# Kernel tuning notes

Measured on AMD Instinct MI355X. Metric: run time of the kernel, lower is better.

The kernel has to match this reference:

```python
import jax, jax.numpy as jnp
import numpy as np

EMBED = 1024
HEADS = 16
HEAD_DIM = EMBED // HEADS
HIDDEN = 4 * EMBED
EPS = 1e-5


def setup_inputs() -> dict:
    key = jax.random.key(0)
    ks = jax.random.split(key, 9)
    s = lambda fan_in: 1.0 / np.sqrt(fan_in)
    inp = {
        "x": jax.random.normal(ks[0], (2, 2048, EMBED), dtype=jnp.float32),
        "ln1_w": jnp.ones((EMBED,), jnp.float32),
        "ln1_b": jnp.zeros((EMBED,), jnp.float32),
        "ln2_w": jnp.ones((EMBED,), jnp.float32),
        "ln2_b": jnp.zeros((EMBED,), jnp.float32),
        "qkv_w": jax.random.uniform(ks[1], (EMBED, 3 * EMBED), jnp.float32, -s(EMBED), s(EMBED)),
        "qkv_b": jax.random.uniform(ks[2], (3 * EMBED,), jnp.float32, -s(EMBED), s(EMBED)),
        "proj_w": jax.random.uniform(ks[3], (EMBED, EMBED), jnp.float32, -s(EMBED), s(EMBED)),
        "proj_b": jax.random.uniform(ks[4], (EMBED,), jnp.float32, -s(EMBED), s(EMBED)),
        "fc1_w": jax.random.uniform(ks[5], (EMBED, HIDDEN), jnp.float32, -s(EMBED), s(EMBED)),
        "fc1_b": jax.random.uniform(ks[6], (HIDDEN,), jnp.float32, -s(EMBED), s(EMBED)),
        "fc2_w": jax.random.uniform(ks[7], (HIDDEN, EMBED), jnp.float32, -s(HIDDEN), s(HIDDEN)),
        "fc2_b": jax.random.uniform(ks[8], (EMBED,), jnp.float32, -s(HIDDEN), s(HIDDEN)),
    }
    return inp


def _layernorm(x, w, b):
    mu = jnp.mean(x, axis=-1, keepdims=True)
    var = jnp.mean(jnp.square(x - mu), axis=-1, keepdims=True)
    return (x - mu) * jax.lax.rsqrt(var + EPS) * w + b


def _attn(x, qkv_w, qkv_b, proj_w, proj_b):
    B, N, C = x.shape
    qkv = x @ qkv_w + qkv_b                      # [B,N,3C]
    qkv = qkv.reshape(B, N, 3, HEADS, HEAD_DIM)
    q, k, v = qkv[:, :, 0], qkv[:, :, 1], qkv[:, :, 2]   # [B,N,H,D]
    scale = HEAD_DIM ** -0.5
    scores = jnp.einsum("bqhd,bkhd->bhqk", q, k) * scale  # [B,H,N,N]
    attn = jax.nn.softmax(scores, axis=-1)
    out = jnp.einsum("bhqk,bkhd->bqhd", attn, v).reshape(B, N, C)
    return out @ proj_w + proj_b


def _mlp(x, fc1_w, fc1_b, fc2_w, fc2_b):
    h = jax.nn.gelu(x @ fc1_w + fc1_b, approximate=False)
    return h @ fc2_w + fc2_b


def reference(x, ln1_w, ln1_b, ln2_w, ln2_b, qkv_w, qkv_b, proj_w, proj_b,
              fc1_w, fc1_b, fc2_w, fc2_b):
    # pre-norm transformer block (eval mode: dropout/drop_path are identity)
    x = x + _attn(_layernorm(x, ln1_w, ln1_b), qkv_w, qkv_b, proj_w, proj_b)
    x = x + _mlp(_layernorm(x, ln2_w, ln2_b), fc1_w, fc1_b, fc2_w, fc2_b)
    return x
```

## Files before the change

### kernel.cpp

```cpp
#include <hip/hip_runtime.h>
#include <hip/hip_bf16.h>

#define SEQ    2048
#define BATCH  2
#define MTOK   4096
#define EMBED  1024
#define HEADS  16
#define HDIM   64
#define QKV3   3072
#define FFN    4096

typedef __attribute__((ext_vector_type(8))) short bf16x8;
typedef __attribute__((ext_vector_type(4))) float f32x4;

static __device__ __forceinline__ unsigned short f2bf(float f) {
  union { float f; unsigned u; } x; x.f = f;
  unsigned r = x.u + 0x7FFFu + ((x.u >> 16) & 1u);
  return (unsigned short)(r >> 16);
}
static __device__ __forceinline__ float bf2f(unsigned short u) {
  union { unsigned u; float f; } x; x.u = ((unsigned)u) << 16; return x.f;
}
static __device__ __forceinline__ unsigned pk2bf(float a, float b) {
#if __has_builtin(__builtin_amdgcn_cvt_pk_bf16_f32)
  typedef __attribute__((ext_vector_type(2))) __bf16 bf16x2_t;
  union { bf16x2_t v; unsigned u; } x;
  x.v = __builtin_amdgcn_cvt_pk_bf16_f32(a, b);
  return x.u;
#else
  return ((unsigned)f2bf(a)) | (((unsigned)f2bf(b)) << 16);
#endif
}
static __device__ __forceinline__ float fexp2(float x) {
#if __has_builtin(__builtin_amdgcn_exp2f)
  return __builtin_amdgcn_exp2f(x);
#else
  return exp2f(x);
#endif
}
static __device__ __forceinline__ float frcp(float x) {
#if __has_builtin(__builtin_amdgcn_rcpf)
  return __builtin_amdgcn_rcpf(x);
#else
  return 1.0f / x;
#endif
}
static __device__ __forceinline__ float fgelu(float v) {
  float t = v * v;
  float z = v * __builtin_fmaf(-0.1029456f, t, -2.3022650687f);
  return v * frcp(1.0f + fexp2(z));
}

static __device__ __forceinline__ void gload16(const unsigned short* g, unsigned short* l) {
  __builtin_amdgcn_global_load_lds((const __attribute__((address_space(1))) void*)g,
                                   (__attribute__((address_space(3))) void*)l, 16, 0, 0);
}

struct TD { const float* W; unsigned short* T; int K, N, ntx, base; };
struct TD4 { TD d[4]; };

__global__ void transpose_all(TD4 td) {
  __shared__ float t[32][33];
  int bid = blockIdx.x;
  int i = 0;
  if (bid >= td.d[1].base) i = 1;
  if (bid >= td.d[2].base) i = 2;
  if (bid >= td.d[3].base) i = 3;
  const TD& D = td.d[i];
  int local = bid - D.base;
  int n0 = (local % D.ntx) * 32, k0 = (local / D.ntx) * 32;
  int tx = threadIdx.x, ty = threadIdx.y;
#pragma unroll
  for (int j = 0; j < 32; j += 8)
    t[ty + j][tx] = D.W[(size_t)(k0 + ty + j) * D.N + n0 + tx];
  __syncthreads();
#pragma unroll
  for (int j = 0; j < 32; j += 8)
    D.T[(size_t)(n0 + ty + j) * D.K + k0 + tx] = f2bf(t[tx][ty + j]);
}

__global__ __launch_bounds__(256) void ln_kernel(const float* __restrict__ in,
                                                 const float* __restrict__ w,
                                                 const float* __restrict__ b,
                                                 unsigned short* __restrict__ out) {
  __shared__ float sh[4];
  int row = blockIdx.x, tid = threadIdx.x;
  const float4 v = ((const float4*)(in + (size_t)row * EMBED))[tid];
  float s = v.x + v.y + v.z + v.w;
#pragma unroll
  for (int off = 32; off; off >>= 1) s += __shfl_xor(s, off);
  if ((tid & 63) == 0) sh[tid >> 6] = s;
  __syncthreads();
  float mean = (sh[0] + sh[1] + sh[2] + sh[3]) * (1.0f / EMBED);
  __syncthreads();
  float dx = v.x - mean, dy = v.y - mean, dz = v.z - mean, dw = v.w - mean;
  float q = dx * dx + dy * dy + dz * dz + dw * dw;
#pragma unroll
  for (int off = 32; off; off >>= 1) q += __shfl_xor(q, off);
  if ((tid & 63) == 0) sh[tid >> 6] = q;
  __syncthreads();
  float var = (sh[0] + sh[1] + sh[2] + sh[3]) * (1.0f / EMBED);
  float rs = rsqrtf(var + 1e-5f);
  const float4 wv = ((const float4*)w)[tid];
  const float4 bv = ((const float4*)b)[tid];
  ushort4 o;
  o.x = f2bf(dx * rs * wv.x + bv.x);
  o.y = f2bf(dy * rs * wv.y + bv.y);
  o.z = f2bf(dz * rs * wv.z + bv.z);
  o.w = f2bf(dw * rs * wv.w + bv.w);
  ((ushort4*)(out + (size_t)row * EMBED))[tid] = o;
}

template <int ACT, int OUTBF, int VSPLIT>
__global__ __launch_bounds__(256) void gemmBig(const unsigned short* __restrict__ A,
                                               const unsigned short* __restrict__ Wt,
                                               const float* __restrict__ bias,
                                               unsigned short* __restrict__ outB,
                                               float* __restrict__ outF,
                                               unsigned short* __restrict__ vT,
                                               int M, int N, int K, int nblk) {
  __shared__ __align__(16) unsigned short As[128 * 64];
  __shared__ __align__(16) unsigned short Bs[128 * 64];
  const int tid = threadIdx.x;
  const int wave = tid >> 6, lane = tid & 63;
  const int quad = lane >> 4, ml = lane & 15;
  const int wr = wave >> 1, wc = wave & 1;
  const int m0 = (blockIdx.x / nblk) * 128;
  const int n0 = (blockIdx.x % nblk) * 128;
  const int srow = lane >> 3;
  const int schunk = (lane & 7) ^ (srow & 7);
  const unsigned short* Ag = A + (size_t)(m0 + wave * 32 + srow) * K + schunk * 8;
  const unsigned short* Bg = Wt + (size_t)(n0 + wave * 32 + srow) * K + schunk * 8;
  unsigned short* AsW = &As[wave * 2048];
  unsigned short* BsW = &Bs[wave * 2048];
  f32x4 acc[4][4];
#pragma unroll
  for (int i = 0; i < 4; i++)
#pragma unroll
    for (int j = 0; j < 4; j++) acc[i][j] = (f32x4){0.f, 0.f, 0.f, 0.f};
  for (int k0 = 0; k0 < K; k0 += 64) {
    __syncthreads();
#pragma unroll
    for (int t = 0; t < 4; t++) {
      gload16(Ag + (size_t)(8 * t) * K, AsW + 512 * t);
      gload16(Bg + (size_t)(8 * t) * K, BsW + 512 * t);
    }
    Ag += 64; Bg += 64;
    __syncthreads();
#pragma unroll
    for (int kh = 0; kh < 2; kh++) {
      const int ch = ((kh * 4 + quad) ^ (ml & 7)) * 8;
      bf16x8 af[4], bfr[4];
#pragma unroll
      for (int mt = 0; mt < 4; mt++)
        af[mt] = *(const bf16x8*)&As[(wr * 64 + mt * 16 + ml) * 64 + ch];
#pragma unroll
      for (int nt = 0; nt < 4; nt++)
        bfr[nt] = *(const bf16x8*)&Bs[(wc * 64 + nt * 16 + ml) * 64 + ch];
#pragma unroll
      for (int mt = 0; mt < 4; mt++)
#pragma unroll
        for (int nt = 0; nt < 4; nt++)
          acc[mt][nt] = __builtin_amdgcn_mfma_f32_16x16x32_bf16(af[mt], bfr[nt], acc[mt][nt], 0, 0, 0);
    }
  }
#pragma unroll
  for (int mt = 0; mt < 4; mt++)
#pragma unroll
    for (int nt = 0; nt < 4; nt++) {
      const int col0 = n0 + wc * 64 + nt * 16;
      const int row0 = m0 + wr * 64 + mt * 16;
      if (VSPLIT && col0 >= 2 * EMBED) {
        const int b = row0 >> 11, tok0 = row0 & (SEQ - 1);
        const int h = (col0 - 2 * EMBED) >> 6;
        const int dl = ((col0 - 2 * EMBED) & 63) + ml;
        float bia = bias[col0 + ml];
        ushort4 o;
        o.x = f2bf(acc[mt][nt][0] + bia);
        o.y = f2bf(acc[mt][nt][1] + bia);
        o.z = f2bf(acc[mt][nt][2] + bia);
        o.w = f2bf(acc[mt][nt][3] + bia);
        *(ushort4*)(vT + (size_t)((b * 16 + h) * 64 + dl) * SEQ + tok0 + quad * 4) = o;
      } else {
#pragma unroll
        for (int r = 0; r < 4; r++) {
          int row = row0 + quad * 4 + r;
          int col = col0 + ml;
          float v = acc[mt][nt][r] + bias[col];
          if (ACT) v = fgelu(v);
          if (OUTBF)
            outB[(size_t)row * N + col] = f2bf(v);
          else
            outF[(size_t)row * N + col] = v;
        }
      }
    }
}

template <int RES, int OUTBF>
__global__ __launch_bounds__(256) void gemm64k(const unsigned short* __restrict__ A,
                                               const unsigned short* __restrict__ Wt,
                                               const float* __restrict__ bias,
                                               const float* __restrict__ res,
                                               unsigned short* __restrict__ outB,
                                               float* __restrict__ outF,
                                               int M, int N, int K, int nblk) {
  __shared__ __align__(16) unsigned short As[2][128 * 64];
  __shared__ __align__(16) unsigned short Bs[2][64 * 64];
  const int tid = threadIdx.x;
  const int wave = tid >> 6, lane = tid & 63;
  const int quad = lane >> 4, ml = lane & 15;
  const int wr = wave >> 1, wc = wave & 1;
  const int xcd = blockIdx.x & 7, idx = blockIdx.x >> 3;
  const int mPerXcd = (gridDim.x >> 3) / nblk;
  const int m0 = (xcd * mPerXcd + idx / nblk) * 128;
  const int n0 = (idx % nblk) * 64;
  const int srow = lane >> 3;
  const int schunk = (lane & 7) ^ (srow & 7);
  const unsigned short* Ag = A + (size_t)(m0 + wave * 32 + srow) * K + schunk * 8;
  const unsigned short* Bg = Wt + (size_t)(n0 + wave * 16 + srow) * K + schunk * 8;
  f32x4 acc[4][2];
#pragma unroll
  for (int i = 0; i < 4; i++) { acc[i][0] = (f32x4){0.f,0.f,0.f,0.f}; acc[i][1] = acc[i][0]; }
  {
    unsigned short* AsW = &As[0][wave * 2048];
    unsigned short* BsW = &Bs[0][wave * 1024];
    gload16(Ag, AsW);
    gload16(Ag + (size_t)8 * K,  AsW + 512);
    gload16(Ag + (size_t)16 * K, AsW + 1024);
    gload16(Ag + (size_t)24 * K, AsW + 1536);
    gload16(Bg, BsW);
    gload16(Bg + (size_t)8 * K,  BsW + 512);
    Ag += 64; Bg += 64;
  }
  __syncthreads();
  const int nk = K >> 6;
  for (int kk = 0; kk < nk; ++kk) {
    const int cur = kk & 1;
    if (kk + 1 < nk) {
      unsigned short* AsW = &As[cur ^ 1][wave * 2048];
      unsigned short* BsW = &Bs[cur ^ 1][wave * 1024];
      gload16(Ag, AsW);
      gload16(Ag + (size_t)8 * K,  AsW + 512);
      gload16(Ag + (size_t)16 * K, AsW + 1024);
      gload16(Ag + (size_t)24 * K, AsW + 1536);
      gload16(Bg, BsW);
      gload16(Bg + (size_t)8 * K,  BsW + 512);
      Ag += 64; Bg += 64;
    }
#pragma unroll
    for (int kh = 0; kh < 2; kh++) {
      const int ch = ((kh * 4 + quad) ^ (ml & 7)) * 8;
      bf16x8 af[4], bfr[2];
#pragma unroll
      for (int mt = 0; mt < 4; mt++)
        af[mt] = *(const bf16x8*)&As[cur][(wr * 64 + mt * 16 + ml) * 64 + ch];
#pragma unroll
      for (int nt = 0; nt < 2; nt++)
        bfr[nt] = *(const bf16x8*)&Bs[cur][(wc * 32 + nt * 16 + ml) * 64 + ch];
#pragma unroll
      for (int mt = 0; mt < 4; mt++)
#pragma unroll
        for (int nt = 0; nt < 2; nt++)
          acc[mt][nt] = __builtin_amdgcn_mfma_f32_16x16x32_bf16(af[mt], bfr[nt], acc[mt][nt], 0, 0, 0);
    }
    __syncthreads();
  }
#pragma unroll
  for (int mt = 0; mt < 4; mt++)
#pragma unroll
    for (int nt = 0; nt < 2; nt++)
#pragma unroll
      for (int r = 0; r < 4; r++) {
        int row = m0 + wr * 64 + mt * 16 + quad * 4 + r;
        int col = n0 + wc * 32 + nt * 16 + ml;
        float v = acc[mt][nt][r] + bias[col];
        if (RES) v += res[(size_t)row * N + col];
        if (OUTBF)
          outB[(size_t)row * N + col] = f2bf(v);
        else
          outF[(size_t)row * N + col] = v;
      }
}

__global__ __launch_bounds__(256) void attn_kernel(const unsigned short* __restrict__ qkv,
                                                   const unsigned short* __restrict__ vT,
                                                   unsigned short* __restrict__ attn) {
  __shared__ __align__(16) unsigned short Ks[2][64 * 64];
  __shared__ __align__(16) unsigned short Vs[2][64 * 64];
  __shared__ __align__(16) unsigned short Ps[4][16 * 64];
  const int tid = threadIdx.x, wave = tid >> 6, lane = tid & 63;
  const int quad = lane >> 4, ml = lane & 15;
  const int bh = blockIdx.x, b = bh >> 4, h = bh & 15;
  const int q0 = blockIdx.y * 64 + wave * 16;
  const float qscale = 0.18033688011112042f;
  const unsigned short* qrow = qkv + (size_t)(b * SEQ + q0 + ml) * QKV3 + h * HDIM;
  bf16x8 aq0 = *(const bf16x8*)(qrow + quad * 8);
  bf16x8 aq1 = *(const bf16x8*)(qrow + 32 + quad * 8);
#pragma unroll
  for (int j = 0; j < 8; j++) {
    aq0[j] = (short)f2bf(bf2f((unsigned short)aq0[j]) * qscale);
    aq1[j] = (short)f2bf(bf2f((unsigned short)aq1[j]) * qscale);
  }
  bf16x8 ones;
#pragma unroll
  for (int j = 0; j < 8; j++) ones[j] = (short)0x3F80;
  f32x4 O[4], lsum = {0.f, 0.f, 0.f, 0.f};
#pragma unroll
  for (int i = 0; i < 4; i++) O[i] = (f32x4){0.f, 0.f, 0.f, 0.f};
  const int skey = lane >> 3;
  const int schunk8 = (((lane & 7) ^ ((lane >> 3) & 7))) * 8;
  const int swz = (ml & 7);
  const unsigned short* kbase =
      qkv + (size_t)(b * SEQ + wave * 16 + skey) * QKV3 + EMBED + h * HDIM + schunk8;
  const unsigned short* vbase =
      vT + (size_t)(bh * 64 + wave * 16 + skey) * SEQ + schunk8;
  unsigned short* PsW = &Ps[wave][0];

  gload16(kbase, &Ks[0][wave * 1024]);
  gload16(kbase + (size_t)8 * QKV3, &Ks[0][wave * 1024] + 512);
  gload16(vbase, &Vs[0][wave * 1024]);
  gload16(vbase + (size_t)8 * SEQ, &Vs[0][wave * 1024] + 512);
  __syncthreads();

  for (int kti = 0; kti < SEQ / 64; ++kti) {
    const int cur = kti & 1;
    if (kti + 1 < SEQ / 64) {
      const int kt = (kti + 1) * 64;
      unsigned short* kd = &Ks[cur ^ 1][wave * 1024];
      unsigned short* vd = &Vs[cur ^ 1][wave * 1024];
      gload16(kbase + (size_t)kt * QKV3, kd);
      gload16(kbase + (size_t)(kt + 8) * QKV3, kd + 512);
      gload16(vbase + kt, vd);
      gload16(vbase + kt + (size_t)8 * SEQ, vd + 512);
    }
    const unsigned short* Kc = &Ks[cur][0];
    const unsigned short* Vc = &Vs[cur][0];
#pragma unroll
    for (int s = 0; s < 4; s++) {
      bf16x8 blo = *(const bf16x8*)&Kc[(s * 16 + ml) * 64 + (quad ^ swz) * 8];
      bf16x8 bhi = *(const bf16x8*)&Kc[(s * 16 + ml) * 64 + ((4 + quad) ^ swz) * 8];
      f32x4 St = {0.f, 0.f, 0.f, 0.f};
      St = __builtin_amdgcn_mfma_f32_16x16x32_bf16(blo, aq0, St, 0, 0, 0);
      St = __builtin_amdgcn_mfma_f32_16x16x32_bf16(bhi, aq1, St, 0, 0, 0);
      uint2 pk_;
      pk_.x = pk2bf(fexp2(St[0]), fexp2(St[1]));
      pk_.y = pk2bf(fexp2(St[2]), fexp2(St[3]));
      const int chs = (2 * s + (quad >> 1)) ^ swz;
      *(uint2*)((char*)PsW + ml * 128 + chs * 16 + (quad & 1) * 8) = pk_;
    }
    bf16x8 ap0 = *(const bf16x8*)((const char*)PsW + ml * 128 + ((quad ^ swz) << 4));
    bf16x8 ap1 = *(const bf16x8*)((const char*)PsW + ml * 128 + (((4 + quad) ^ swz) << 4));
    __builtin_amdgcn_s_setprio(1);
    lsum = __builtin_amdgcn_mfma_f32_16x16x32_bf16(ap0, ones, lsum, 0, 0, 0);
    lsum = __builtin_amdgcn_mfma_f32_16x16x32_bf16(ap1, ones, lsum, 0, 0, 0);
#pragma unroll
    for (int d = 0; d < 4; d++) {
      bf16x8 bv0 = *(const bf16x8*)&Vc[(d * 16 + ml) * 64 + (quad ^ swz) * 8];
      bf16x8 bv1 = *(const bf16x8*)&Vc[(d * 16 + ml) * 64 + ((4 + quad) ^ swz) * 8];
      O[d] = __builtin_amdgcn_mfma_f32_16x16x32_bf16(ap0, bv0, O[d], 0, 0, 0);
      O[d] = __builtin_amdgcn_mfma_f32_16x16x32_bf16(ap1, bv1, O[d], 0, 0, 0);
    }
    __builtin_amdgcn_s_setprio(0);
    __syncthreads();
  }
#pragma unroll
  for (int r = 0; r < 4; r++) {
    float inv = 1.0f / lsum[r];
    size_t g = (size_t)(b * SEQ + q0 + quad * 4 + r) * EMBED + h * HDIM + ml;
    attn[g + 0]  = f2bf(O[0][r] * inv);
    attn[g + 16] = f2bf(O[1][r] * inv);
    attn[g + 32] = f2bf(O[2][r] * inv);
    attn[g + 48] = f2bf(O[3][r] * inv);
  }
}

extern "C" void kernel_launch(void* const* d_in, const int* in_sizes, int n_in,
                              void* d_out, int out_size, void* d_ws, size_t ws_size,
                              hipStream_t stream) {
  const float* x      = (const float*)d_in[0];
  const float* ln1_w  = (const float*)d_in[1];
  const float* ln1_b  = (const float*)d_in[2];
  const float* ln2_w  = (const float*)d_in[3];
  const float* ln2_b  = (const float*)d_in[4];
  const float* qkv_w  = (const float*)d_in[5];
  const float* qkv_b  = (const float*)d_in[6];
  const float* proj_w = (const float*)d_in[7];
  const float* proj_b = (const float*)d_in[8];
  const float* fc1_w  = (const float*)d_in[9];
  const float* fc1_b  = (const float*)d_in[10];
  const float* fc2_w  = (const float*)d_in[11];
  const float* fc2_b  = (const float*)d_in[12];
  float* out = (float*)d_out;
  char* wsb = (char*)d_ws;
  unsigned short* lnbuf  = (unsigned short*)(wsb + 0);
  unsigned short* qkvb   = (unsigned short*)(wsb + 8388608);
  unsigned short* attnb  = (unsigned short*)(wsb + 33554432);
  unsigned short* vTb    = (unsigned short*)(wsb + 41943040);
  unsigned short* actb   = (unsigned short*)(wsb + 33554432);
  float*          h1     = (float*)(wsb + 67108864);
  unsigned short* qkvWt  = (unsigned short*)(wsb + 83886080);
  unsigned short* projWt = (unsigned short*)(wsb + 90177536);
  unsigned short* fc1Wt  = (unsigned short*)(wsb + 92274688);
  unsigned short* fc2Wt  = (unsigned short*)(wsb + 100663296);

  TD4 td;
  td.d[0] = {qkv_w,  qkvWt,  1024, 3072,  96, 0};
  td.d[1] = {proj_w, projWt, 1024, 1024,  32, 3072};
  td.d[2] = {fc1_w,  fc1Wt,  1024, 4096, 128, 4096};
  td.d[3] = {fc2_w,  fc2Wt,  4096, 1024,  32, 8192};
  transpose_all<<<12288, dim3(32, 8), 0, stream>>>(td);

  ln_kernel<<<MTOK, 256, 0, stream>>>(x, ln1_w, ln1_b, lnbuf);
  gemmBig<0, 1, 1><<<768, 256, 0, stream>>>(
      lnbuf, qkvWt, qkv_b, qkvb, nullptr, vTb, MTOK, QKV3, EMBED, 24);
  attn_kernel<<<dim3(32, 32), 256, 0, stream>>>(qkvb, vTb, attnb);
  gemm64k<1, 0><<<512, 256, 0, stream>>>(
      attnb, projWt, proj_b, x, nullptr, h1, MTOK, EMBED, EMBED, 16);
  ln_kernel<<<MTOK, 256, 0, stream>>>(h1, ln2_w, ln2_b, lnbuf);
  gemmBig<1, 1, 0><<<1024, 256, 0, stream>>>(
      lnbuf, fc1Wt, fc1_b, actb, nullptr, nullptr, MTOK, FFN, EMBED, 32);
  gemm64k<1, 0><<<512, 256, 0, stream>>>(
      actb, fc2Wt, fc2_b, h1, nullptr, out, MTOK, EMBED, FFN, 16);
}
```

Measured before the change: 348.6 us.

## Rewrite attention with 32x32x16 MFMA, 32 queries per wave, shuffle-based P transpose

Attention now uses 32x32x16 bf16 MFMA tiles, with each wave handling 32 query rows, so each block covers 128 queries and the grid is halved. The exponentiated scores are moved into the A-operand layout with cross-half-wave shuffles instead of a round trip through LDS, which removes the P shared buffer. Each K/V tile loaded into LDS is reused across twice as many queries. The cost is more accumulator registers (three 16-float accumulators plus the scores) under launch_bounds(256,2), and fewer blocks overall.

```diff
diff --git a/kernel.cpp b/kernel.cpp
--- a/kernel.cpp
+++ b/kernel.cpp
@@ -12,6 +12,7 @@
 
 typedef __attribute__((ext_vector_type(8))) short bf16x8;
 typedef __attribute__((ext_vector_type(4))) float f32x4;
+typedef __attribute__((ext_vector_type(16))) float f32x16;
 
 static __device__ __forceinline__ unsigned short f2bf(float f) {
   union { float f; unsigned u; } x; x.f = f;
@@ -283,39 +284,42 @@
       }
 }
 
-__global__ __launch_bounds__(256) void attn_kernel(const unsigned short* __restrict__ qkv,
-                                                   const unsigned short* __restrict__ vT,
-                                                   unsigned short* __restrict__ attn) {
+__global__ __launch_bounds__(256, 2) void attn_kernel(const unsigned short* __restrict__ qkv,
+                                                      const unsigned short* __restrict__ vT,
+                                                      unsigned short* __restrict__ attn) {
   __shared__ __align__(16) unsigned short Ks[2][64 * 64];
   __shared__ __align__(16) unsigned short Vs[2][64 * 64];
-  __shared__ __align__(16) unsigned short Ps[4][16 * 64];
   const int tid = threadIdx.x, wave = tid >> 6, lane = tid & 63;
-  const int quad = lane >> 4, ml = lane & 15;
+  const int l31 = lane & 31, hi = lane >> 5;
   const int bh = blockIdx.x, b = bh >> 4, h = bh & 15;
-  const int q0 = blockIdx.y * 64 + wave * 16;
+  const int q0w = blockIdx.y * 128 + wave * 32;
   const float qscale = 0.18033688011112042f;
-  const unsigned short* qrow = qkv + (size_t)(b * SEQ + q0 + ml) * QKV3 + h * HDIM;
-  bf16x8 aq0 = *(const bf16x8*)(qrow + quad * 8);
-  bf16x8 aq1 = *(const bf16x8*)(qrow + 32 + quad * 8);
-#pragma unroll
-  for (int j = 0; j < 8; j++) {
-    aq0[j] = (short)f2bf(bf2f((unsigned short)aq0[j]) * qscale);
-    aq1[j] = (short)f2bf(bf2f((unsigned short)aq1[j]) * qscale);
+  const int sw = l31 & 7;
+
+  const unsigned short* qrow = qkv + (size_t)(b * SEQ + q0w + l31) * QKV3 + h * HDIM;
+  bf16x8 bq[4];
+#pragma unroll
+  for (int s = 0; s < 4; s++) {
+    bq[s] = *(const bf16x8*)(qrow + s * 16 + hi * 8);
+#pragma unroll
+    for (int j = 0; j < 8; j++)
+      bq[s][j] = (short)f2bf(bf2f((unsigned short)bq[s][j]) * qscale);
   }
   bf16x8 ones;
 #pragma unroll
   for (int j = 0; j < 8; j++) ones[j] = (short)0x3F80;
-  f32x4 O[4], lsum = {0.f, 0.f, 0.f, 0.f};
-#pragma unroll
-  for (int i = 0; i < 4; i++) O[i] = (f32x4){0.f, 0.f, 0.f, 0.f};
+
+  f32x16 zz;
+#pragma unroll
+  for (int i = 0; i < 16; i++) zz[i] = 0.f;
+  f32x16 O0 = zz, O1 = zz, lsum = zz;
+
   const int skey = lane >> 3;
-  const int schunk8 = (((lane & 7) ^ ((lane >> 3) & 7))) * 8;
-  const int swz = (ml & 7);
+  const int schunk8 = ((lane & 7) ^ (skey & 7)) * 8;
   const unsigned short* kbase =
       qkv + (size_t)(b * SEQ + wave * 16 + skey) * QKV3 + EMBED + h * HDIM + schunk8;
   const unsigned short* vbase =
       vT + (size_t)(bh * 64 + wave * 16 + skey) * SEQ + schunk8;
-  unsigned short* PsW = &Ps[wave][0];
 
   gload16(kbase, &Ks[0][wave * 1024]);
   gload16(kbase + (size_t)8 * QKV3, &Ks[0][wave * 1024] + 512);
@@ -336,42 +340,63 @@
     }
     const unsigned short* Kc = &Ks[cur][0];
     const unsigned short* Vc = &Vs[cur][0];
+
+    f32x16 St0 = zz, St1 = zz;
 #pragma unroll
     for (int s = 0; s < 4; s++) {
-      bf16x8 blo = *(const bf16x8*)&Kc[(s * 16 + ml) * 64 + (quad ^ swz) * 8];
-      bf16x8 bhi = *(const bf16x8*)&Kc[(s * 16 + ml) * 64 + ((4 + quad) ^ swz) * 8];
-      f32x4 St = {0.f, 0.f, 0.f, 0.f};
-      St = __builtin_amdgcn_mfma_f32_16x16x32_bf16(blo, aq0, St, 0, 0, 0);
-      St = __builtin_amdgcn_mfma_f32_16x16x32_bf16(bhi, aq1, St, 0, 0, 0);
-      uint2 pk_;
-      pk_.x = pk2bf(fexp2(St[0]), fexp2(St[1]));
-      pk_.y = pk2bf(fexp2(St[2]), fexp2(St[3]));
-      const int chs = (2 * s + (quad >> 1)) ^ swz;
-      *(uint2*)((char*)PsW + ml * 128 + chs * 16 + (quad & 1) * 8) = pk_;
-    }
-    bf16x8 ap0 = *(const bf16x8*)((const char*)PsW + ml * 128 + ((quad ^ swz) << 4));
-    bf16x8 ap1 = *(const bf16x8*)((const char*)PsW + ml * 128 + (((4 + quad) ^ swz) << 4));
+      bf16x8 ak0 = *(const bf16x8*)&Kc[l31 * 64 + (((2 * s + hi) ^ sw)) * 8];
+      bf16x8 ak1 = *(const bf16x8*)&Kc[(32 + l31) * 64 + (((2 * s + hi) ^ sw)) * 8];
+      St0 = __builtin_amdgcn_mfma_f32_32x32x16_bf16(ak0, bq[s], St0, 0, 0, 0);
+      St1 = __builtin_amdgcn_mfma_f32_32x32x16_bf16(ak1, bq[s], St1, 0, 0, 0);
+    }
+
+    unsigned W0[2][4], W1[2][4];
+#pragma unroll
+    for (int g = 0; g < 4; g++) {
+      W0[0][g] = pk2bf(fexp2(St0[4 * g]), fexp2(St0[4 * g + 1]));
+      W1[0][g] = pk2bf(fexp2(St0[4 * g + 2]), fexp2(St0[4 * g + 3]));
+      W0[1][g] = pk2bf(fexp2(St1[4 * g]), fexp2(St1[4 * g + 1]));
+      W1[1][g] = pk2bf(fexp2(St1[4 * g + 2]), fexp2(St1[4 * g + 3]));
+    }
+
+    bf16x8 pa[4];
+#pragma unroll
+    for (int ks = 0; ks < 4; ks++) {
+      const int kt2 = ks >> 1, g0 = 2 * (ks & 1), g1 = g0 + 1;
+      unsigned send0 = hi ? W0[kt2][g0] : W0[kt2][g1];
+      unsigned send1 = hi ? W1[kt2][g0] : W1[kt2][g1];
+      unsigned recv0 = __shfl_xor((int)send0, 32);
+      unsigned recv1 = __shfl_xor((int)send1, 32);
+      union { unsigned u[4]; bf16x8 v; } pw;
+      pw.u[0] = hi ? recv0 : W0[kt2][g0];
+      pw.u[1] = hi ? recv1 : W1[kt2][g0];
+      pw.u[2] = hi ? W0[kt2][g1] : recv0;
+      pw.u[3] = hi ? W1[kt2][g1] : recv1;
+      pa[ks] = pw.v;
+    }
+
     __builtin_amdgcn_s_setprio(1);
-    lsum = __builtin_amdgcn_mfma_f32_16x16x32_bf16(ap0, ones, lsum, 0, 0, 0);
-    lsum = __builtin_amdgcn_mfma_f32_16x16x32_bf16(ap1, ones, lsum, 0, 0, 0);
-#pragma unroll
-    for (int d = 0; d < 4; d++) {
-      bf16x8 bv0 = *(const bf16x8*)&Vc[(d * 16 + ml) * 64 + (quad ^ swz) * 8];
-      bf16x8 bv1 = *(const bf16x8*)&Vc[(d * 16 + ml) * 64 + ((4 + quad) ^ swz) * 8];
-      O[d] = __builtin_amdgcn_mfma_f32_16x16x32_bf16(ap0, bv0, O[d], 0, 0, 0);
-      O[d] = __builtin_amdgcn_mfma_f32_16x16x32_bf16(ap1, bv1, O[d], 0, 0, 0);
+#pragma unroll
+    for (int ks = 0; ks < 4; ks++)
+      lsum = __builtin_amdgcn_mfma_f32_32x32x16_bf16(pa[ks], ones, lsum, 0, 0, 0);
+#pragma unroll
+    for (int ks = 0; ks < 4; ks++) {
+      bf16x8 bv0 = *(const bf16x8*)&Vc[l31 * 64 + (((2 * ks + hi) ^ sw)) * 8];
+      bf16x8 bv1 = *(const bf16x8*)&Vc[(32 + l31) * 64 + (((2 * ks + hi) ^ sw)) * 8];
+      O0 = __builtin_amdgcn_mfma_f32_32x32x16_bf16(pa[ks], bv0, O0, 0, 0, 0);
+      O1 = __builtin_amdgcn_mfma_f32_32x32x16_bf16(pa[ks], bv1, O1, 0, 0, 0);
     }
     __builtin_amdgcn_s_setprio(0);
     __syncthreads();
   }
-#pragma unroll
-  for (int r = 0; r < 4; r++) {
+
+#pragma unroll
+  for (int r = 0; r < 16; r++) {
+    const int qr = (r & 3) + 8 * (r >> 2) + 4 * hi;
     float inv = 1.0f / lsum[r];
-    size_t g = (size_t)(b * SEQ + q0 + quad * 4 + r) * EMBED + h * HDIM + ml;
-    attn[g + 0]  = f2bf(O[0][r] * inv);
-    attn[g + 16] = f2bf(O[1][r] * inv);
-    attn[g + 32] = f2bf(O[2][r] * inv);
-    attn[g + 48] = f2bf(O[3][r] * inv);
+    size_t g = (size_t)(b * SEQ + q0w + qr) * EMBED + h * HDIM + l31;
+    attn[g]      = f2bf(O0[r] * inv);
+    attn[g + 32] = f2bf(O1[r] * inv);
   }
 }
 
@@ -414,7 +439,7 @@
   ln_kernel<<<MTOK, 256, 0, stream>>>(x, ln1_w, ln1_b, lnbuf);
   gemmBig<0, 1, 1><<<768, 256, 0, stream>>>(
       lnbuf, qkvWt, qkv_b, qkvb, nullptr, vTb, MTOK, QKV3, EMBED, 24);
-  attn_kernel<<<dim3(32, 32), 256, 0, stream>>>(qkvb, vTb, attnb);
+  attn_kernel<<<dim3(32, 16), 256, 0, stream>>>(qkvb, vTb, attnb);
   gemm64k<1, 0><<<512, 256, 0, stream>>>(
       attnb, projWt, proj_b, x, nullptr, h1, MTOK, EMBED, EMBED, 16);
   ln_kernel<<<MTOK, 256, 0, stream>>>(h1, ln2_w, ln2_b, lnbuf);
```

Measured after the change: 366.1 us. +5.0%, slower.
